# Performance work log

Measured on AMD Instinct MI355X. Metric: run time of the kernel, lower is better.

Reference implementation:

```python
import jax, jax.numpy as jnp
import numpy as np

NLOC = 10  # local nodes per element (cubic DG triangle)


def setup_inputs() -> dict:
    key = jax.random.key(0)
    ks = jax.random.split(key, 6)
    nele, nloc, ngi = 500000, NLOC, 13
    return {
        "r0": jax.random.normal(ks[0], (nele * nloc,), dtype=jnp.float32),
        "c_i": jax.random.normal(ks[1], (nele * nloc,), dtype=jnp.float32),
        "c_n": jax.random.normal(ks[2], (nele, 1, nloc), dtype=jnp.float32),
        "k": jnp.ones((1,), dtype=jnp.float32),
        "dt": jnp.ones((1,), dtype=jnp.float32),
        "n": jax.random.normal(ks[3], (nloc, ngi), dtype=jnp.float32),
        "nx": jax.random.normal(ks[4], (nele, 2, nloc, ngi), dtype=jnp.float32),
        "detwei": jax.random.uniform(ks[5], (nele, ngi), dtype=jnp.float32),
    }


def reference(r0, c_i, c_n, k, dt, n, nx, detwei):
    nele, _, nloc, ngi = nx.shape
    c_i = c_i.reshape(nele, 1, nloc)               # [e,1,l]
    # stiffness: sum over spatial dims of grad-grad quadrature contraction
    nx1nx1 = jnp.einsum('eig,ejg,eg->eij', nx[:, 0], nx[:, 0], detwei)
    nx2nx2 = jnp.einsum('eig,ejg,eg->eij', nx[:, 1], nx[:, 1], detwei)
    nxnx = (nx1nx1 + nx2nx2) * k                   # [e,i,j] * [1]
    # mass matrix per element (shared shape funcs, per-element detwei)
    nn = jnp.einsum('ig,jg,eg->eij', n, n, detwei)
    # transient branch (config.isTransient = True)
    nn_dt = nn / dt
    nxnx = nn_dt + nxnx
    r0 = r0.reshape(nele, nloc, 1)
    r0 = r0 + jnp.matmul(nn_dt, jnp.swapaxes(c_n, 1, 2))   # [e,i,1]
    r0 = r0.reshape(-1)
    r0 = r0 - jnp.matmul(nxnx, jnp.swapaxes(c_i, 1, 2)).reshape(-1)
    diagA = jnp.diagonal(nxnx, axis1=-2, axis2=-1)          # [e,nloc]
    bdiagA = nxnx
    return (bdiagA, diagA, r0)
```

## Files before the change

kernel.cpp:

```cpp
#include <hip/hip_runtime.h>

#define NLOC  10
#define NGI   13
#define NPAIR 55
#define EPB   64
#define TPB   256

#define W_NX   0
#define W_DW   16640
#define W_N    17472
#define W_TOT  17604

#define NX_GRAN  4160
#define TOT_GRAN 4368

typedef float vf2 __attribute__((ext_vector_type(2)));

__device__ __forceinline__ constexpr int pidx(int i, int j) {
    return i * NLOC - (i * (i - 1)) / 2 + (j - i);
}

__device__ __forceinline__ void stage16(const float* gsrc, float* lds) {
    __builtin_amdgcn_global_load_lds(
        (const __attribute__((address_space(1))) void*)gsrc,
        (__attribute__((address_space(3))) void*)lds, 16, 0, 0);
}

__global__ __launch_bounds__(TPB) void fem_kernel(
    const float* __restrict__ r0g,
    const float* __restrict__ cig,
    const float* __restrict__ cng,
    const float* __restrict__ kp,
    const float* __restrict__ dtp,
    const float* __restrict__ nmat,
    const float* __restrict__ nx,
    const float* __restrict__ dwei,
    float* __restrict__ out,
    int nele)
{
    __shared__ float sm[W_TOT];

    const int  t   = threadIdx.x;
    const long e0  = (long)blockIdx.x * EPB;
    const int  rem = min(EPB, nele - (int)e0);

    const float* nxsrc = nx   + (size_t)e0 * 260;
    const float* dwsrc = dwei + (size_t)e0 * 13;
    const int capnx = rem * 260;
    const int capdw = rem * 13;
    float* ldsb = sm + (t >> 6) * 256;
    #pragma unroll
    for (int k = 0; k < 18; ++k) {
        const int G = k * 256 + t;
        if (G < NX_GRAN) {
            if (G * 4 < capnx) stage16(nxsrc + (size_t)G * 4, ldsb + k * 1024);
        } else if (G < TOT_GRAN) {
            const int rel = G - NX_GRAN;
            if (rel * 4 < capdw) stage16(dwsrc + (size_t)rel * 4, ldsb + k * 1024);
        }
    }
    if (t < 130) sm[W_N + t] = nmat[t];
    __syncthreads();

    const int  eloc = t >> 2;
    const int  d    = (t >> 1) & 1;
    const int  h    = t & 1;
    const int  q    = t & 3;
    const long e    = e0 + eloc;
    const bool live = eloc < rem;
    const long ee   = live ? e : (long)(nele - 1);

    const float kk  = kp[0];
    const float idt = 1.0f / dtp[0];

    const float* smnx = sm + eloc * 260 + d * 130;
    const float* smdw = sm + W_DW + eloc * 13;
    const float* smn  = sm + W_N;

    float civ[NLOC], dif[NLOC];
    {
        const vf2* ci2 = reinterpret_cast<const vf2*>(cig + (size_t)ee * 10);
        const vf2* cn2 = reinterpret_cast<const vf2*>(cng + (size_t)ee * 10);
        #pragma unroll
        for (int u2 = 0; u2 < 5; ++u2) {
            vf2 a = ci2[u2], b = cn2[u2];
            civ[2*u2]   = a.x; civ[2*u2+1] = a.y;
            dif[2*u2]   = b.x - a.x; dif[2*u2+1] = b.y - a.y;
        }
    }

    float acc[NPAIR];
    #pragma unroll
    for (int p = 0; p < NPAIR; ++p) acc[p] = 0.0f;
    float r0a[NLOC];
    #pragma unroll
    for (int i = 0; i < NLOC; ++i) r0a[i] = 0.0f;

    #pragma unroll
    for (int it = 0; it < 7; ++it) {
        const int   graw = 2 * it + h;
        const int   g    = graw < NGI ? graw : NGI - 1;
        const float wv   = graw < NGI ? kk * smdw[g] : 0.0f;
        float col[NLOC];
        #pragma unroll
        for (int l = 0; l < NLOC; ++l) col[l] = smnx[l * 13 + g];
        float u = 0.0f;
        #pragma unroll
        for (int l = 0; l < NLOC; ++l) u = fmaf(col[l], civ[l], u);
        const float uw = u * wv;
        #pragma unroll
        for (int i = 0; i < NLOC; ++i) {
            const float ti = col[i] * wv;
            #pragma unroll
            for (int j = i; j < NLOC; ++j)
                acc[pidx(i, j)] = fmaf(ti, col[j], acc[pidx(i, j)]);
            r0a[i] = fmaf(-col[i], uw, r0a[i]);
        }
    }

    #pragma unroll
    for (int it = 0; it < 4; ++it) {
        const int   graw = q + 4 * it;
        const int   g    = graw < NGI ? graw : NGI - 1;
        const float wv   = graw < NGI ? idt * smdw[g] : 0.0f;
        float ncol[NLOC];
        #pragma unroll
        for (int l = 0; l < NLOC; ++l) ncol[l] = smn[l * 13 + g];
        float wd = 0.0f;
        #pragma unroll
        for (int l = 0; l < NLOC; ++l) wd = fmaf(ncol[l], dif[l], wd);
        #pragma unroll
        for (int i = 0; i < NLOC; ++i) {
            const float ti = ncol[i] * wv;
            #pragma unroll
            for (int j = i; j < NLOC; ++j)
                acc[pidx(i, j)] = fmaf(ti, ncol[j], acc[pidx(i, j)]);
            r0a[i] = fmaf(ti, wd, r0a[i]);
        }
    }

    #pragma unroll
    for (int p = 0; p < NPAIR; ++p) {
        acc[p] += __shfl_xor(acc[p], 1);
        acc[p] += __shfl_xor(acc[p], 2);
    }
    #pragma unroll
    for (int i = 0; i < NLOC; ++i) {
        r0a[i] += __shfl_xor(r0a[i], 1);
        r0a[i] += __shfl_xor(r0a[i], 2);
    }

    if (live) {
        float* obd = out + (size_t)e * 100;
        float* odg = out + (size_t)nele * 100 + (size_t)e * 10;
        float* oro = out + (size_t)nele * 110 + (size_t)e * 10;
        const float* r0s = r0g + (size_t)e * 10;
        #pragma unroll
        for (int i = 0; i < NLOC; ++i) {
            if ((i & 3) == q) {
                float row[NLOC];
                #pragma unroll
                for (int j = 0; j < NLOC; ++j) {
                    const int lo = i < j ? i : j, hi = i < j ? j : i;
                    row[j] = acc[pidx(lo, hi)];
                }
                #pragma unroll
                for (int u2 = 0; u2 < 5; ++u2) {
                    vf2 v = { row[2*u2], row[2*u2+1] };
                    *reinterpret_cast<vf2*>(obd + i * 10 + 2 * u2) = v;
                }
                odg[i] = row[i];
                oro[i] = r0s[i] + r0a[i];
            }
        }
    }
}

extern "C" void kernel_launch(void* const* d_in, const int* in_sizes, int n_in,
                              void* d_out, int out_size, void* d_ws, size_t ws_size,
                              hipStream_t stream) {
    const float* r0   = (const float*)d_in[0];
    const float* ci   = (const float*)d_in[1];
    const float* cn   = (const float*)d_in[2];
    const float* k    = (const float*)d_in[3];
    const float* dt   = (const float*)d_in[4];
    const float* nmat = (const float*)d_in[5];
    const float* nx   = (const float*)d_in[6];
    const float* dw   = (const float*)d_in[7];
    const int nele = in_sizes[7] / NGI;

    const int nb = (nele + EPB - 1) / EPB;
    fem_kernel<<<nb, TPB, 0, stream>>>(r0, ci, cn, k, dt, nmat, nx, dw,
                                       (float*)d_out, nele);
}
```

Before: 209.3 us.

## Convert to persistent grid with double-buffered LDS prefetch of next chunk

The kernel becomes persistent: the grid is capped at 256 blocks, and each block loops over 64-element chunks. It prefetches the next chunk's nx and detwei into a second LDS buffer with async global-to-LDS loads while it computes the current chunk. The goal is to overlap global-memory staging with compute and to avoid per-block launch and stage-then-wait serialization. The cost is that LDS per block roughly doubles, to about 140KB. That limits a CU to a single block of 4 waves, so memory latency hiding through occupancy is reduced.

```diff
diff --git a/kernel.cpp b/kernel.cpp
--- a/kernel.cpp
+++ b/kernel.cpp
@@ -6,10 +6,9 @@
 #define EPB   64
 #define TPB   256
 
-#define W_NX   0
-#define W_DW   16640
-#define W_N    17472
-#define W_TOT  17604
+#define BUF_FL   17472
+#define W_N      (2 * BUF_FL)
+#define W_TOT    (W_N + 130)
 
 #define NX_GRAN  4160
 #define TOT_GRAN 4368
@@ -40,139 +39,157 @@
 {
     __shared__ float sm[W_TOT];
 
-    const int  t   = threadIdx.x;
-    const long e0  = (long)blockIdx.x * EPB;
-    const int  rem = min(EPB, nele - (int)e0);
-
-    const float* nxsrc = nx   + (size_t)e0 * 260;
-    const float* dwsrc = dwei + (size_t)e0 * 13;
-    const int capnx = rem * 260;
-    const int capdw = rem * 13;
-    float* ldsb = sm + (t >> 6) * 256;
-    #pragma unroll
-    for (int k = 0; k < 18; ++k) {
-        const int G = k * 256 + t;
-        if (G < NX_GRAN) {
-            if (G * 4 < capnx) stage16(nxsrc + (size_t)G * 4, ldsb + k * 1024);
-        } else if (G < TOT_GRAN) {
-            const int rel = G - NX_GRAN;
-            if (rel * 4 < capdw) stage16(dwsrc + (size_t)rel * 4, ldsb + k * 1024);
-        }
-    }
+    const int t       = threadIdx.x;
+    const int nchunks = (nele + EPB - 1) / EPB;
+    const int gs      = gridDim.x;
+
     if (t < 130) sm[W_N + t] = nmat[t];
-    __syncthreads();
+
+    auto stage_chunk = [&](int b, int c) {
+        const long ce0   = (long)c * EPB;
+        const int  crem  = min(EPB, nele - (int)ce0);
+        const int  capnx = crem * 260;
+        const int  capdw = crem * 13;
+        const float* nxsrc = nx   + (size_t)ce0 * 260;
+        const float* dwsrc = dwei + (size_t)ce0 * 13;
+        float* ldsb = sm + b * BUF_FL + (t >> 6) * 256;
+        #pragma unroll
+        for (int k = 0; k < 18; ++k) {
+            const int G = k * 256 + t;
+            if (G < NX_GRAN) {
+                if (G * 4 < capnx) stage16(nxsrc + (size_t)G * 4, ldsb + k * 1024);
+            } else if (G < TOT_GRAN) {
+                const int rel = G - NX_GRAN;
+                if (rel * 4 < capdw) stage16(dwsrc + (size_t)rel * 4, ldsb + k * 1024);
+            }
+        }
+    };
 
     const int  eloc = t >> 2;
     const int  d    = (t >> 1) & 1;
     const int  h    = t & 1;
     const int  q    = t & 3;
-    const long e    = e0 + eloc;
-    const bool live = eloc < rem;
-    const long ee   = live ? e : (long)(nele - 1);
-
     const float kk  = kp[0];
     const float idt = 1.0f / dtp[0];
-
-    const float* smnx = sm + eloc * 260 + d * 130;
-    const float* smdw = sm + W_DW + eloc * 13;
-    const float* smn  = sm + W_N;
-
-    float civ[NLOC], dif[NLOC];
-    {
-        const vf2* ci2 = reinterpret_cast<const vf2*>(cig + (size_t)ee * 10);
-        const vf2* cn2 = reinterpret_cast<const vf2*>(cng + (size_t)ee * 10);
-        #pragma unroll
-        for (int u2 = 0; u2 < 5; ++u2) {
-            vf2 a = ci2[u2], b = cn2[u2];
-            civ[2*u2]   = a.x; civ[2*u2+1] = a.y;
-            dif[2*u2]   = b.x - a.x; dif[2*u2+1] = b.y - a.y;
-        }
-    }
-
-    float acc[NPAIR];
-    #pragma unroll
-    for (int p = 0; p < NPAIR; ++p) acc[p] = 0.0f;
-    float r0a[NLOC];
-    #pragma unroll
-    for (int i = 0; i < NLOC; ++i) r0a[i] = 0.0f;
-
-    #pragma unroll
-    for (int it = 0; it < 7; ++it) {
-        const int   graw = 2 * it + h;
-        const int   g    = graw < NGI ? graw : NGI - 1;
-        const float wv   = graw < NGI ? kk * smdw[g] : 0.0f;
-        float col[NLOC];
-        #pragma unroll
-        for (int l = 0; l < NLOC; ++l) col[l] = smnx[l * 13 + g];
-        float u = 0.0f;
-        #pragma unroll
-        for (int l = 0; l < NLOC; ++l) u = fmaf(col[l], civ[l], u);
-        const float uw = u * wv;
+    const float* smn = sm + W_N;
+
+    int c = blockIdx.x;
+    if (c < nchunks) stage_chunk(0, c);
+    __syncthreads();
+
+    int cur = 0;
+    for (; c < nchunks; c += gs) {
+        const int next = c + gs;
+        if (next < nchunks) stage_chunk(cur ^ 1, next);
+        const long e0   = (long)c * EPB;
+        const int  rem  = min(EPB, nele - (int)e0);
+        const long e    = e0 + eloc;
+        const bool live = eloc < rem;
+        const long ee   = live ? e : (long)(nele - 1);
+
+        const float* smnx = sm + cur * BUF_FL + eloc * 260 + d * 130;
+        const float* smdw = sm + cur * BUF_FL + 16640 + eloc * 13;
+
+        float civ[NLOC], dif[NLOC];
+        {
+            const vf2* ci2 = reinterpret_cast<const vf2*>(cig + (size_t)ee * 10);
+            const vf2* cn2 = reinterpret_cast<const vf2*>(cng + (size_t)ee * 10);
+            #pragma unroll
+            for (int u2 = 0; u2 < 5; ++u2) {
+                vf2 a = ci2[u2], b = cn2[u2];
+                civ[2*u2]   = a.x; civ[2*u2+1] = a.y;
+                dif[2*u2]   = b.x - a.x; dif[2*u2+1] = b.y - a.y;
+            }
+        }
+
+        float acc[NPAIR];
+        #pragma unroll
+        for (int p = 0; p < NPAIR; ++p) acc[p] = 0.0f;
+        float r0a[NLOC];
+        #pragma unroll
+        for (int i = 0; i < NLOC; ++i) r0a[i] = 0.0f;
+
+        #pragma unroll
+        for (int it = 0; it < 7; ++it) {
+            const int   graw = 2 * it + h;
+            const int   g    = graw < NGI ? graw : NGI - 1;
+            const float wv   = graw < NGI ? kk * smdw[g] : 0.0f;
+            float col[NLOC];
+            #pragma unroll
+            for (int l = 0; l < NLOC; ++l) col[l] = smnx[l * 13 + g];
+            float u = 0.0f;
+            #pragma unroll
+            for (int l = 0; l < NLOC; ++l) u = fmaf(col[l], civ[l], u);
+            const float uw = u * wv;
+            #pragma unroll
+            for (int i = 0; i < NLOC; ++i) {
+                const float ti = col[i] * wv;
+                #pragma unroll
+                for (int j = i; j < NLOC; ++j)
+                    acc[pidx(i, j)] = fmaf(ti, col[j], acc[pidx(i, j)]);
+                r0a[i] = fmaf(-col[i], uw, r0a[i]);
+            }
+        }
+
+        #pragma unroll
+        for (int it = 0; it < 4; ++it) {
+            const int   graw = q + 4 * it;
+            const int   g    = graw < NGI ? graw : NGI - 1;
+            const float wv   = graw < NGI ? idt * smdw[g] : 0.0f;
+            float ncol[NLOC];
+            #pragma unroll
+            for (int l = 0; l < NLOC; ++l) ncol[l] = smn[l * 13 + g];
+            float wd = 0.0f;
+            #pragma unroll
+            for (int l = 0; l < NLOC; ++l) wd = fmaf(ncol[l], dif[l], wd);
+            #pragma unroll
+            for (int i = 0; i < NLOC; ++i) {
+                const float ti = ncol[i] * wv;
+                #pragma unroll
+                for (int j = i; j < NLOC; ++j)
+                    acc[pidx(i, j)] = fmaf(ti, ncol[j], acc[pidx(i, j)]);
+                r0a[i] = fmaf(ti, wd, r0a[i]);
+            }
+        }
+
+        #pragma unroll
+        for (int p = 0; p < NPAIR; ++p) {
+            acc[p] += __shfl_xor(acc[p], 1);
+            acc[p] += __shfl_xor(acc[p], 2);
+        }
         #pragma unroll
         for (int i = 0; i < NLOC; ++i) {
-            const float ti = col[i] * wv;
-            #pragma unroll
-            for (int j = i; j < NLOC; ++j)
-                acc[pidx(i, j)] = fmaf(ti, col[j], acc[pidx(i, j)]);
-            r0a[i] = fmaf(-col[i], uw, r0a[i]);
-        }
-    }
-
-    #pragma unroll
-    for (int it = 0; it < 4; ++it) {
-        const int   graw = q + 4 * it;
-        const int   g    = graw < NGI ? graw : NGI - 1;
-        const float wv   = graw < NGI ? idt * smdw[g] : 0.0f;
-        float ncol[NLOC];
-        #pragma unroll
-        for (int l = 0; l < NLOC; ++l) ncol[l] = smn[l * 13 + g];
-        float wd = 0.0f;
-        #pragma unroll
-        for (int l = 0; l < NLOC; ++l) wd = fmaf(ncol[l], dif[l], wd);
-        #pragma unroll
-        for (int i = 0; i < NLOC; ++i) {
-            const float ti = ncol[i] * wv;
-            #pragma unroll
-            for (int j = i; j < NLOC; ++j)
-                acc[pidx(i, j)] = fmaf(ti, ncol[j], acc[pidx(i, j)]);
-            r0a[i] = fmaf(ti, wd, r0a[i]);
-        }
-    }
-
-    #pragma unroll
-    for (int p = 0; p < NPAIR; ++p) {
-        acc[p] += __shfl_xor(acc[p], 1);
-        acc[p] += __shfl_xor(acc[p], 2);
-    }
-    #pragma unroll
-    for (int i = 0; i < NLOC; ++i) {
-        r0a[i] += __shfl_xor(r0a[i], 1);
-        r0a[i] += __shfl_xor(r0a[i], 2);
-    }
-
-    if (live) {
-        float* obd = out + (size_t)e * 100;
-        float* odg = out + (size_t)nele * 100 + (size_t)e * 10;
-        float* oro = out + (size_t)nele * 110 + (size_t)e * 10;
-        const float* r0s = r0g + (size_t)e * 10;
-        #pragma unroll
-        for (int i = 0; i < NLOC; ++i) {
-            if ((i & 3) == q) {
-                float row[NLOC];
-                #pragma unroll
-                for (int j = 0; j < NLOC; ++j) {
-                    const int lo = i < j ? i : j, hi = i < j ? j : i;
-                    row[j] = acc[pidx(lo, hi)];
+            r0a[i] += __shfl_xor(r0a[i], 1);
+            r0a[i] += __shfl_xor(r0a[i], 2);
+        }
+
+        if (live) {
+            float* obd = out + (size_t)e * 100;
+            float* odg = out + (size_t)nele * 100 + (size_t)e * 10;
+            float* oro = out + (size_t)nele * 110 + (size_t)e * 10;
+            const float* r0s = r0g + (size_t)e * 10;
+            #pragma unroll
+            for (int i = 0; i < NLOC; ++i) {
+                if ((i & 3) == q) {
+                    float row[NLOC];
+                    #pragma unroll
+                    for (int j = 0; j < NLOC; ++j) {
+                        const int lo = i < j ? i : j, hi = i < j ? j : i;
+                        row[j] = acc[pidx(lo, hi)];
+                    }
+                    #pragma unroll
+                    for (int u2 = 0; u2 < 5; ++u2) {
+                        vf2 v = { row[2*u2], row[2*u2+1] };
+                        *reinterpret_cast<vf2*>(obd + i * 10 + 2 * u2) = v;
+                    }
+                    odg[i] = row[i];
+                    oro[i] = r0s[i] + r0a[i];
                 }
-                #pragma unroll
-                for (int u2 = 0; u2 < 5; ++u2) {
-                    vf2 v = { row[2*u2], row[2*u2+1] };
-                    *reinterpret_cast<vf2*>(obd + i * 10 + 2 * u2) = v;
-                }
-                odg[i] = row[i];
-                oro[i] = r0s[i] + r0a[i];
-            }
-        }
+            }
+        }
+
+        __syncthreads();
+        cur ^= 1;
     }
 }
 
@@ -189,7 +206,8 @@
     const float* dw   = (const float*)d_in[7];
     const int nele = in_sizes[7] / NGI;
 
-    const int nb = (nele + EPB - 1) / EPB;
+    const int nchunks = (nele + EPB - 1) / EPB;
+    const int nb = min(256, nchunks);
     fem_kernel<<<nb, TPB, 0, stream>>>(r0, ci, cn, k, dt, nmat, nx, dw,
                                        (float*)d_out, nele);
 }
```

Result: slower. 249.2 us (+19.1%).
